# Performance work log

Measured on AMD Instinct MI355X. Metric: run time of the kernel, lower is better.

## Reference

```python
import jax, jax.numpy as jnp
import numpy as np
import math

H = 12  # heads (init kwarg)
KEEP_RATE = 0.7  # forward arg keep_rate (< 1 -> token pruning path)


def setup_inputs() -> dict:
    key = jax.random.key(0)
    k0, k1, k2 = jax.random.split(key, 3)
    b, n, c = 32, 577, 768  # ViT-B/16 @ 384px: 576 patches + CLS
    x = jax.random.normal(k0, (b, n, c), dtype=jnp.float32)
    # nn.Linear(dim, dim*3) and nn.Linear(dim, dim); kaiming-ish scale
    W_qkv = jax.random.normal(k1, (c, 3 * c), dtype=jnp.float32) / np.sqrt(c).astype(np.float32)
    b_qkv = jnp.zeros((3 * c,), dtype=jnp.float32)
    W_out = jax.random.normal(k2, (c, c), dtype=jnp.float32) / np.sqrt(c).astype(np.float32)
    b_out = jnp.zeros((c,), dtype=jnp.float32)
    return {"x": x, "keep_rate": KEEP_RATE, "W_qkv": W_qkv, "b_qkv": b_qkv,
            "W_out": W_out, "b_out": b_out}


def reference(x, keep_rate, W_qkv, b_qkv, W_out, b_out):
    b, n, c = x.shape
    d = c // H
    scale = (c / H) ** -0.5
    # qkv projection + split into heads: 'b n (h d) -> b h n d'
    qkv = x @ W_qkv + b_qkv                      # [b, n, 3c]
    q, k, v = jnp.split(qkv, 3, axis=-1)
    split_heads = lambda t: t.reshape(b, n, H, d).transpose(0, 2, 1, 3)
    q, k, v = split_heads(q), split_heads(k), split_heads(v)
    dots = jnp.einsum('bhid,bhjd->bhij', q, k) * scale   # [b,h,n,n]
    attention = jax.nn.softmax(dots, axis=-1)
    out = jnp.einsum('bhij,bhjd->bhid', attention, v)    # [b,h,n,d]
    out = out.transpose(0, 2, 1, 3).reshape(b, n, c)     # 'b h n d -> b n (h d)'
    out = out @ W_out + b_out                            # to_out (dropout=0)
    final_tokens = n - 1
    if keep_rate < 1:
        final_tokens = math.ceil(keep_rate * final_tokens)
        # CLS-token attention to patch tokens, averaged over heads
        class_attention = attention[:, :, 0, 1:].mean(axis=1)   # [b, n-1]
        _, ind = jax.lax.top_k(class_attention, final_tokens)    # [b, final_tokens]
        ind = jnp.sort(ind, axis=1)
        index = jnp.broadcast_to(ind[:, :, None], (b, final_tokens, c))
        return (x, index, ind, class_attention, final_tokens)
    return (out, None, None, None, final_tokens)
```

## Files before the change

kernel.cpp:

```cpp
#include <hip/hip_runtime.h>
#include <math.h>

#define BATCH 32
#define NTOK 577
#define NPATCH 576
#define CDIM 768
#define HEADS 12
#define DHEAD 64
#define W3 2304
#define FT 404

#define WS_WTIL  24576
#define WS_DBIAS 319488
#define WS_DOTS  319872

#define O_X      0ULL
#define O_INDEX  14180352ULL
#define O_IND    24109056ULL
#define O_CA     24121984ULL
#define O_FT     24140416ULL

__global__ __launch_bounds__(512) void k_fold(const float* __restrict__ x,
                                              const float* __restrict__ W,
                                              const float* __restrict__ bq,
                                              float* __restrict__ wtil,
                                              float* __restrict__ dbias) {
    __shared__ float x0s[CDIM];
    __shared__ float red[512];
    __shared__ float qs[DHEAD];
    const int b = blockIdx.x, h = blockIdx.y, tid = threadIdx.x;
    if (tid < CDIM / 4)
        ((float4*)x0s)[tid] = ((const float4*)(x + (size_t)b * NTOK * CDIM))[tid];
    __syncthreads();
    {
        const int d = tid & 63, seg = tid >> 6;
        const float* Wq = W + h * DHEAD + d;
        const int c0 = seg * 96;
        float acc = 0.f;
        #pragma unroll 32
        for (int c = c0; c < c0 + 96; c++) acc += x0s[c] * Wq[(size_t)c * W3];
        red[tid] = acc;
    }
    __syncthreads();
    if (tid < DHEAD) {
        float q = red[tid];
        #pragma unroll
        for (int s = 1; s < 8; s++) q += red[tid + s * 64];
        q += bq[h * DHEAD + tid];
        qs[tid] = q;
        float t = q * bq[CDIM + h * DHEAD + tid];
        #pragma unroll
        for (int off = 32; off; off >>= 1) t += __shfl_down(t, off);
        if (tid == 0) dbias[b * HEADS + h] = t;
    }
    __syncthreads();
    for (int c = tid; c < CDIM; c += 512) {
        const float* wr = W + (size_t)c * W3 + CDIM + h * DHEAD;
        float acc = 0.f;
        #pragma unroll
        for (int d = 0; d < DHEAD; d += 4) {
            float4 a = *reinterpret_cast<const float4*>(wr + d);
            acc += a.x * qs[d] + a.y * qs[d + 1] + a.z * qs[d + 2] + a.w * qs[d + 3];
        }
        wtil[((size_t)b * HEADS + h) * CDIM + c] = acc;
    }
}

#define LOADG(A, G)                                                               \
    {                                                                             \
        _Pragma("unroll")                                                         \
        for (int u = 0; u < 4; u++) {                                             \
            const int j = jbase + (G) * 4 + u;                                    \
            if (j < NTOK) {                                                       \
                const float4* xp =                                                \
                    (const float4*)(x + ((size_t)b * NTOK + j) * CDIM);           \
                A[u][0] = xp[lane]; A[u][1] = xp[64 + lane]; A[u][2] = xp[128 + lane]; \
            } else {                                                              \
                A[u][0] = A[u][1] = A[u][2] = make_float4(0.f, 0.f, 0.f, 0.f);    \
            }                                                                     \
        }                                                                         \
    }

#define COMPG(A, G)                                                               \
    {                                                                             \
        _Pragma("unroll")                                                         \
        for (int u = 0; u < 4; u++) {                                             \
            const int j = jbase + (G) * 4 + u;                                    \
            if (w == u && j < NTOK) {                                             \
                float4* op = (float4*)(out0 + ((size_t)b * NTOK + j) * CDIM);     \
                op[lane] = A[u][0]; op[64 + lane] = A[u][1]; op[128 + lane] = A[u][2]; \
            }                                                                     \
        }                                                                         \
        float acc[4][3];                                                          \
        _Pragma("unroll")                                                         \
        for (int u = 0; u < 4; u++) { acc[u][0] = acc[u][1] = acc[u][2] = 0.f; }  \
        _Pragma("unroll")                                                         \
        for (int i = 0; i < 3; i++)                                               \
            _Pragma("unroll")                                                     \
            for (int u = 0; u < 4; u++)                                           \
                _Pragma("unroll")                                                 \
                for (int hh = 0; hh < 3; hh++)                                    \
                    acc[u][hh] += A[u][i].x * wr[hh][i].x + A[u][i].y * wr[hh][i].y \
                                + A[u][i].z * wr[hh][i].z + A[u][i].w * wr[hh][i].w; \
        _Pragma("unroll")                                                         \
        for (int off = 32; off; off >>= 1)                                        \
            _Pragma("unroll")                                                     \
            for (int u = 0; u < 4; u++)                                           \
                _Pragma("unroll")                                                 \
                for (int hh = 0; hh < 3; hh++)                                    \
                    acc[u][hh] += __shfl_xor(acc[u][hh], off);                    \
        if (lane == 0) {                                                          \
            _Pragma("unroll")                                                     \
            for (int u = 0; u < 4; u++) {                                         \
                const int j = jbase + (G) * 4 + u;                                \
                if (j < NTOK) {                                                   \
                    _Pragma("unroll")                                             \
                    for (int hh = 0; hh < 3; hh++)                                \
                        dots[((size_t)b * HEADS + h0 + hh) * NTOK + j] =          \
                            0.125f * (acc[u][hh] + db[hh]);                       \
                }                                                                 \
            }                                                                     \
        }                                                                         \
    }

__global__ __launch_bounds__(256, 3) void k_dots(const float* __restrict__ x,
                                                 const float* __restrict__ wtil,
                                                 const float* __restrict__ dbias,
                                                 float* __restrict__ dots,
                                                 float* __restrict__ out0) {
    const int b = blockIdx.x, tid = threadIdx.x;
    const int w = tid >> 6, lane = tid & 63, h0 = w * 3;
    float4 wr[3][3];
    float db[3];
    #pragma unroll
    for (int hh = 0; hh < 3; hh++) {
        #pragma unroll
        for (int i = 0; i < 3; i++)
            wr[hh][i] = *reinterpret_cast<const float4*>(
                wtil + ((size_t)b * HEADS + h0 + hh) * CDIM + i * 256 + lane * 4);
        db[hh] = dbias[b * HEADS + h0 + hh];
    }
    const int jbase = blockIdx.y * 16;
    float4 abuf[4][3], nbuf[4][3];
    LOADG(abuf, 0);
    LOADG(nbuf, 1);
    COMPG(abuf, 0);
    LOADG(abuf, 2);
    COMPG(nbuf, 1);
    LOADG(nbuf, 3);
    COMPG(abuf, 2);
    COMPG(nbuf, 3);
}

__global__ __launch_bounds__(512) void k_catbc(const float* __restrict__ dots,
                                               float* __restrict__ out,
                                               int write_ft) {
    __shared__ float dl[HEADS * NTOK];
    __shared__ float mh[HEADS], sh[HEADS];
    __shared__ unsigned vals[NPATCH];
    __shared__ unsigned long long segmask[9];
    __shared__ int segoff[9];
    __shared__ int ind_lds[FT];
    const int b = blockIdx.x, y = blockIdx.y, tid = threadIdx.x;
    {
        const float4* s4 = (const float4*)(dots + (size_t)b * HEADS * NTOK);
        float4* d4 = (float4*)dl;
        for (int i = tid; i < HEADS * NTOK / 4; i += 512) d4[i] = s4[i];
    }
    __syncthreads();
    const int w = tid >> 6, lane = tid & 63;
    for (int h = w; h < HEADS; h += 8) {
        const float* row = dl + h * NTOK;
        float m = -3.4e38f;
        for (int j = lane; j < NTOK; j += 64) m = fmaxf(m, row[j]);
        #pragma unroll
        for (int off = 32; off; off >>= 1) m = fmaxf(m, __shfl_xor(m, off));
        float s = 0.f;
        for (int j = lane; j < NTOK; j += 64) s += expf(row[j] - m);
        #pragma unroll
        for (int off = 32; off; off >>= 1) s += __shfl_xor(s, off);
        if (lane == 0) { mh[h] = m; sh[h] = s; }
    }
    __syncthreads();
    for (int t = tid; t < NPATCH; t += 512) {
        float ca = 0.f;
        #pragma unroll
        for (int h = 0; h < HEADS; h++)
            ca += expf(dl[h * NTOK + 1 + t] - mh[h]) / sh[h];
        ca *= (1.f / 12.f);
        if (y == 0) out[O_CA + (size_t)b * NPATCH + t] = ca;
        vals[t] = __float_as_uint(ca);
    }
    __syncthreads();
    {
        const uint4* v4 = (const uint4*)vals;
        for (int s = w; s < 9; s += 8) {
            const int t = s * 64 + lane;
            const unsigned myv = vals[t];
            int rank = 0;
            #pragma unroll 8
            for (int j4 = 0; j4 < NPATCH / 4; j4++) {
                const uint4 vv = v4[j4];
                const int j = j4 * 4;
                rank += (vv.x > myv) || (vv.x == myv && j     < t);
                rank += (vv.y > myv) || (vv.y == myv && j + 1 < t);
                rank += (vv.z > myv) || (vv.z == myv && j + 2 < t);
                rank += (vv.w > myv) || (vv.w == myv && j + 3 < t);
            }
            const unsigned long long mask = __ballot(rank < FT);
            if (lane == 0) segmask[s] = mask;
        }
    }
    __syncthreads();
    if (tid == 0) {
        int acc = 0;
        #pragma unroll
        for (int s = 0; s < 9; s++) { segoff[s] = acc; acc += __popcll(segmask[s]); }
    }
    __syncthreads();
    for (int s = w; s < 9; s += 8) {
        const int t = s * 64 + lane;
        const unsigned long long mask = segmask[s];
        if ((mask >> lane) & 1ull) {
            const int pos = segoff[s] + __popcll(mask & ((1ull << lane) - 1ull));
            ind_lds[pos] = t;
            if (y == 0) out[O_IND + (size_t)b * FT + pos] = (float)t;
        }
    }
    if (y == 0 && b == 0 && tid == 0 && write_ft) out[O_FT] = (float)FT;
    __syncthreads();
    {
        const int nrows = (FT - 1 - y) / 16 + 1;
        const int total = nrows * 192;
        for (int f = tid; f < total; f += 512) {
            const int k = f / 192, cc = f - k * 192;
            const int r = y + k * 16;
            const float v = (float)ind_lds[r];
            float4 o; o.x = v; o.y = v; o.z = v; o.w = v;
            ((float4*)(out + O_INDEX + ((size_t)b * FT + r) * CDIM))[cc] = o;
        }
    }
}

extern "C" void kernel_launch(void* const* d_in, const int* in_sizes, int n_in,
                              void* d_out, int out_size, void* d_ws, size_t ws_size,
                              hipStream_t stream) {
    const float* x  = (const float*)d_in[0];
    const float* W  = (const float*)d_in[2];
    const float* bq = (const float*)d_in[3];
    float* ws = (float*)d_ws;
    float* out = (float*)d_out;

    k_fold<<<dim3(BATCH, HEADS), 512, 0, stream>>>(x, W, bq, ws + WS_WTIL, ws + WS_DBIAS);
    k_dots<<<dim3(BATCH, 37), 256, 0, stream>>>(x, ws + WS_WTIL, ws + WS_DBIAS,
                                                ws + WS_DOTS, out + O_X);
    const int write_ft = (out_size > (int)O_FT) ? 1 : 0;
    k_catbc<<<dim3(BATCH, 16), 512, 0, stream>>>(ws + WS_DOTS, out, write_ft);
}
```

Measured before the change: 234.0 us.

## Split x copy and index broadcast into a separate flat streaming kernel

Measured after the change: 236.5 us. Within noise of the previous version (+1.0%).

```diff
diff --git a/kernel.cpp b/kernel.cpp
--- a/kernel.cpp
+++ b/kernel.cpp
@@ -13,12 +13,16 @@
 #define WS_WTIL  24576
 #define WS_DBIAS 319488
 #define WS_DOTS  319872
+#define WS_IND   541440
 
 #define O_X      0ULL
 #define O_INDEX  14180352ULL
 #define O_IND    24109056ULL
 #define O_CA     24121984ULL
 #define O_FT     24140416ULL
+
+#define NIDX4  2482176
+#define NCOPY4 3545088
 
 __global__ __launch_bounds__(512) void k_fold(const float* __restrict__ x,
                                               const float* __restrict__ W,
@@ -83,14 +87,6 @@
 
 #define COMPG(A, G)                                                               \
     {                                                                             \
-        _Pragma("unroll")                                                         \
-        for (int u = 0; u < 4; u++) {                                             \
-            const int j = jbase + (G) * 4 + u;                                    \
-            if (w == u && j < NTOK) {                                             \
-                float4* op = (float4*)(out0 + ((size_t)b * NTOK + j) * CDIM);     \
-                op[lane] = A[u][0]; op[64 + lane] = A[u][1]; op[128 + lane] = A[u][2]; \
-            }                                                                     \
-        }                                                                         \
         float acc[4][3];                                                          \
         _Pragma("unroll")                                                         \
         for (int u = 0; u < 4; u++) { acc[u][0] = acc[u][1] = acc[u][2] = 0.f; }  \
@@ -126,8 +122,7 @@
 __global__ __launch_bounds__(256, 3) void k_dots(const float* __restrict__ x,
                                                  const float* __restrict__ wtil,
                                                  const float* __restrict__ dbias,
-                                                 float* __restrict__ dots,
-                                                 float* __restrict__ out0) {
+                                                 float* __restrict__ dots) {
     const int b = blockIdx.x, tid = threadIdx.x;
     const int w = tid >> 6, lane = tid & 63, h0 = w * 3;
     float4 wr[3][3];
@@ -152,16 +147,16 @@
     COMPG(nbuf, 3);
 }
 
-__global__ __launch_bounds__(512) void k_catbc(const float* __restrict__ dots,
-                                               float* __restrict__ out,
-                                               int write_ft) {
+__global__ __launch_bounds__(512) void k_catopk(const float* __restrict__ dots,
+                                                float* __restrict__ out,
+                                                int* __restrict__ indws,
+                                                int write_ft) {
     __shared__ float dl[HEADS * NTOK];
     __shared__ float mh[HEADS], sh[HEADS];
     __shared__ unsigned vals[NPATCH];
     __shared__ unsigned long long segmask[9];
     __shared__ int segoff[9];
-    __shared__ int ind_lds[FT];
-    const int b = blockIdx.x, y = blockIdx.y, tid = threadIdx.x;
+    const int b = blockIdx.x, tid = threadIdx.x;
     {
         const float4* s4 = (const float4*)(dots + (size_t)b * HEADS * NTOK);
         float4* d4 = (float4*)dl;
@@ -188,7 +183,7 @@
         for (int h = 0; h < HEADS; h++)
             ca += expf(dl[h * NTOK + 1 + t] - mh[h]) / sh[h];
         ca *= (1.f / 12.f);
-        if (y == 0) out[O_CA + (size_t)b * NPATCH + t] = ca;
+        out[O_CA + (size_t)b * NPATCH + t] = ca;
         vals[t] = __float_as_uint(ca);
     }
     __syncthreads();
@@ -223,21 +218,29 @@
         const unsigned long long mask = segmask[s];
         if ((mask >> lane) & 1ull) {
             const int pos = segoff[s] + __popcll(mask & ((1ull << lane) - 1ull));
-            ind_lds[pos] = t;
-            if (y == 0) out[O_IND + (size_t)b * FT + pos] = (float)t;
-        }
-    }
-    if (y == 0 && b == 0 && tid == 0 && write_ft) out[O_FT] = (float)FT;
-    __syncthreads();
-    {
-        const int nrows = (FT - 1 - y) / 16 + 1;
-        const int total = nrows * 192;
-        for (int f = tid; f < total; f += 512) {
-            const int k = f / 192, cc = f - k * 192;
-            const int r = y + k * 16;
-            const float v = (float)ind_lds[r];
+            indws[b * FT + pos] = t;
+            out[O_IND + (size_t)b * FT + pos] = (float)t;
+        }
+    }
+    if (b == 0 && tid == 0 && write_ft) out[O_FT] = (float)FT;
+}
+
+__global__ __launch_bounds__(256) void k_bcast(const int* __restrict__ ind,
+                                               const float* __restrict__ x,
+                                               float* __restrict__ out) {
+    const float4* x4 = (const float4*)x;
+    float4* o4 = (float4*)(out + O_X);
+    float4* i4 = (float4*)(out + O_INDEX);
+    const unsigned stride = gridDim.x * 256u;
+    for (unsigned g = blockIdx.x * 256u + threadIdx.x; g < NIDX4 + NCOPY4; g += stride) {
+        if (g < NCOPY4) {
+            o4[g] = x4[g];
+        } else {
+            const unsigned e = g - NCOPY4;
+            const unsigned row = e / 192u;
+            const float v = (float)ind[row];
             float4 o; o.x = v; o.y = v; o.z = v; o.w = v;
-            ((float4*)(out + O_INDEX + ((size_t)b * FT + r) * CDIM))[cc] = o;
+            i4[e] = o;
         }
     }
 }
@@ -253,7 +256,8 @@
 
     k_fold<<<dim3(BATCH, HEADS), 512, 0, stream>>>(x, W, bq, ws + WS_WTIL, ws + WS_DBIAS);
     k_dots<<<dim3(BATCH, 37), 256, 0, stream>>>(x, ws + WS_WTIL, ws + WS_DBIAS,
-                                                ws + WS_DOTS, out + O_X);
+                                                ws + WS_DOTS);
     const int write_ft = (out_size > (int)O_FT) ? 1 : 0;
-    k_catbc<<<dim3(BATCH, 16), 512, 0, stream>>>(ws + WS_DOTS, out, write_ft);
-}
+    k_catopk<<<BATCH, 512, 0, stream>>>(ws + WS_DOTS, out, (int*)(ws + WS_IND), write_ft);
+    k_bcast<<<2048, 256, 0, stream>>>((const int*)(ws + WS_IND), x, out);
+}
```
